# Kernel optimization log

Measured on AMD Instinct MI355X. Metric: run time of the kernel, lower is better.

## Reference

```python
import jax, jax.numpy as jnp
import numpy as np

N = 100000
E = 3200000
G = 64  # number of graphs in the batch


def gat_layer(x, edge_index, edge_attr, W, a_src, a_dst, We, a_e, b, n):
    """Single-head PyG GATConv with edge features.
    add_self_loops=True, fill_value='mean', negative_slope=0.2.
    Returns (out [n,C], new_edge_index [2,E+n], alpha [E+n,1])."""
    src, dst = edge_index[0], edge_index[1]
    # self-loop edge_attr = mean of incoming edge attrs (fill_value='mean')
    deg = jax.ops.segment_sum(jnp.ones_like(dst, dtype=edge_attr.dtype), dst, n)
    loop_attr = jax.ops.segment_sum(edge_attr, dst, n) / jnp.maximum(deg, 1.0)[:, None]
    loop = jnp.arange(n, dtype=src.dtype)
    src = jnp.concatenate([src, loop])
    dst = jnp.concatenate([dst, loop])
    ea = jnp.concatenate([edge_attr, loop_attr], axis=0)  # [E+n, edge_dim]
    h = x @ W                                             # [n, C]
    asrc = h @ a_src                                      # [n]
    adst = h @ a_dst                                      # [n]
    ae = (ea @ We) @ a_e                                  # [E+n]
    alpha = jax.nn.leaky_relu(asrc[src] + adst[dst] + ae, negative_slope=0.2)
    # segment softmax over destination nodes (every node has a self-loop)
    amax = jax.ops.segment_max(alpha, dst, n)
    ex = jnp.exp(alpha - amax[dst])
    denom = jax.ops.segment_sum(ex, dst, n)
    alpha = ex / (denom[dst] + 1e-16)
    out = jax.ops.segment_sum(alpha[:, None] * h[src], dst, n) + b
    return out, jnp.stack([src, dst]), alpha[:, None]


def setup_inputs() -> dict:
    key = jax.random.key(0)
    ks = jax.random.split(key, 24)
    s = 0.1
    inp = {
        "x": jax.random.normal(ks[0], (N, 5), jnp.float32),
        "edge_index": jax.random.randint(ks[1], (2, E), 0, N, jnp.int32),
        "edge_attr": jax.random.normal(ks[2], (E, 3), jnp.float32),
        "batch": jnp.sort(jax.random.randint(ks[3], (N,), 0, G, jnp.int32)),
        # conv1: in=5 -> 64, edge_dim=3
        "W1": jax.random.normal(ks[4], (5, 64), jnp.float32) * s,
        "as1": jax.random.normal(ks[5], (64,), jnp.float32) * s,
        "ad1": jax.random.normal(ks[6], (64,), jnp.float32) * s,
        "We1": jax.random.normal(ks[7], (3, 64), jnp.float32) * s,
        "ae1": jax.random.normal(ks[8], (64,), jnp.float32) * s,
        "b1": jnp.zeros((64,), jnp.float32),
        # conv2: 64 -> 64, edge_dim=1
        "W2": jax.random.normal(ks[9], (64, 64), jnp.float32) * s,
        "as2": jax.random.normal(ks[10], (64,), jnp.float32) * s,
        "ad2": jax.random.normal(ks[11], (64,), jnp.float32) * s,
        "We2": jax.random.normal(ks[12], (1, 64), jnp.float32) * s,
        "ae2": jax.random.normal(ks[13], (64,), jnp.float32) * s,
        "b2": jnp.zeros((64,), jnp.float32),
        # conv3: 64 -> 32, edge_dim=1
        "W3": jax.random.normal(ks[14], (64, 32), jnp.float32) * s,
        "as3": jax.random.normal(ks[15], (32,), jnp.float32) * s,
        "ad3": jax.random.normal(ks[16], (32,), jnp.float32) * s,
        "We3": jax.random.normal(ks[17], (1, 32), jnp.float32) * s,
        "ae3": jax.random.normal(ks[18], (32,), jnp.float32) * s,
        "b3": jnp.zeros((32,), jnp.float32),
    }
    return inp


def reference(x, edge_index, edge_attr, batch,
              W1, as1, ad1, We1, ae1, b1,
              W2, as2, ad2, We2, ae2, b2,
              W3, as3, ad3, We3, ae3, b3):
    h, ei, alpha = gat_layer(x, edge_index, edge_attr, W1, as1, ad1, We1, ae1, b1, N)
    h = jax.nn.relu(h)
    h, ei, alpha = gat_layer(h, ei, alpha, W2, as2, ad2, We2, ae2, b2, N)
    h = jax.nn.relu(h)
    h, _, _ = gat_layer(h, ei, alpha, W3, as3, ad3, We3, ae3, b3, N)
    # global mean pool over graphs
    cnt = jax.ops.segment_sum(jnp.ones((N,), h.dtype), batch, G)
    out = jax.ops.segment_sum(h, batch, G) / jnp.maximum(cnt, 1.0)[:, None]
    return out  # [G, 32]
```

## Files before the change

### kernel.cpp

```cpp
#include <hip/hip_runtime.h>
#include <hip/hip_fp16.h>

#define LRELU(x) ((x) > 0.f ? (x) : 0.2f * (x))
#define SBSH 9
#define SBN 512
#define NB1 256
#define MAXSB 1024
#define PC 16

__global__ void small_weights_k(const float* __restrict__ We1, const float* __restrict__ ae1,
                                const float* __restrict__ We2, const float* __restrict__ ae2,
                                const float* __restrict__ We3, const float* __restrict__ ae3,
                                float* __restrict__ sw) {
  int t = threadIdx.x;
  float v0 = We1[t] * ae1[t];
  float v1 = We1[64 + t] * ae1[t];
  float v2 = We1[128 + t] * ae1[t];
  float v3 = We2[t] * ae2[t];
  float v4 = (t < 32) ? We3[t] * ae3[t] : 0.f;
#pragma unroll
  for (int off = 32; off > 0; off >>= 1) {
    v0 += __shfl_down(v0, off);
    v1 += __shfl_down(v1, off);
    v2 += __shfl_down(v2, off);
    v3 += __shfl_down(v3, off);
    v4 += __shfl_down(v4, off);
  }
  if (t == 0) { sw[0] = v0; sw[1] = v1; sw[2] = v2; sw[3] = v3; sw[4] = v4; }
}

__global__ __launch_bounds__(256) void count1_k(const int* __restrict__ dst,
                                                int* __restrict__ gcnt, int E, int NSB) {
  __shared__ int cnt[MAXSB];
  const int t = threadIdx.x, blk = blockIdx.x;
  for (int i = t; i < NSB; i += 256) cnt[i] = 0;
  __syncthreads();
  const int CE = (E + NB1 - 1) / NB1;
  const int e0 = blk * CE, e1 = min(E, e0 + CE);
  for (int e = e0 + t; e < e1; e += 256) {
    int d = __builtin_nontemporal_load(&dst[e]);
    atomicAdd(&cnt[d >> SBSH], 1);
  }
  __syncthreads();
  for (int i = t; i < NSB; i += 256) gcnt[i * NB1 + blk] = cnt[i];
}

__global__ __launch_bounds__(1024) void scanA_k(const int* __restrict__ gcnt,
                                                int* __restrict__ gbase,
                                                int* __restrict__ bsum, int M) {
  __shared__ int s[1024];
  const int t = threadIdx.x;
  const int i = blockIdx.x * 1024 + t;
  int v = (i < M) ? gcnt[i] : 0;
  s[t] = v;
  __syncthreads();
  for (int off = 1; off < 1024; off <<= 1) {
    int add = (t >= off) ? s[t - off] : 0;
    __syncthreads();
    s[t] += add;
    __syncthreads();
  }
  if (i < M) gbase[i] = s[t] - v;
  if (t == 1023) bsum[blockIdx.x] = s[t];
}

__global__ void scanB_k(const int* __restrict__ bsum, int* __restrict__ boff, int nb) {
  if (threadIdx.x == 0) {
    int acc = 0;
    for (int b = 0; b < nb; b++) { boff[b] = acc; acc += bsum[b]; }
  }
}

__global__ void scanC_k(int* __restrict__ gbase, const int* __restrict__ boff,
                        int* __restrict__ rowptr, int M, int E) {
  int i = blockIdx.x * 256 + threadIdx.x;
  if (i < M) gbase[i] += boff[i >> 10];
  if (i == 0) { gbase[M] = E; rowptr[0] = 0; }
}

__global__ __launch_bounds__(256) void append2_k(
    const int* __restrict__ src, const int* __restrict__ dst,
    const float* __restrict__ eattr, const int* __restrict__ gbase,
    int2* __restrict__ recDS, const float* __restrict__ sw, int E, int NSB) {
  __shared__ int base[MAXSB];
  __shared__ int off[MAXSB];
  const int t = threadIdx.x, blk = blockIdx.x;
  for (int i = t; i < NSB; i += 256) { base[i] = gbase[i * NB1 + blk]; off[i] = 0; }
  __syncthreads();
  const float w0 = sw[0], w1 = sw[1], w2 = sw[2];
  const int CE = (E + NB1 - 1) / NB1;
  const int e0 = blk * CE, e1 = min(E, e0 + CE);
  for (int e = e0 + t; e < e1; e += 256) {
    int d = __builtin_nontemporal_load(&dst[e]);
    int sv = __builtin_nontemporal_load(&src[e]);
    float a0 = __builtin_nontemporal_load(&eattr[e * 3]);
    float a1 = __builtin_nontemporal_load(&eattr[e * 3 + 1]);
    float a2 = __builtin_nontemporal_load(&eattr[e * 3 + 2]);
    float ae = a0 * w0 + a1 * w1 + a2 * w2;
    int sb = d >> SBSH;
    int pos = base[sb] + atomicAdd(&off[sb], 1);
    recDS[pos] = make_int2((int)(((unsigned)(d & (SBN - 1)) << 23) | (unsigned)sv),
                           __float_as_int(ae));
  }
}

__global__ __launch_bounds__(1024) void sb_build_k(
    const int2* __restrict__ recDS, const int* __restrict__ gbase,
    const float* __restrict__ asrc, const float* __restrict__ adst,
    int* __restrict__ rowptr, float* __restrict__ asum, float* __restrict__ esum,
    int2* __restrict__ edge, int n, int NSB) {
  __shared__ int cnt[SBN];
  __shared__ int sc[SBN];
  __shared__ int fill[SBN];
  __shared__ float adl[SBN];
  __shared__ float rs[SBN];
  __shared__ float es[SBN];
  const int t = threadIdx.x, sb = blockIdx.x;
  const int v0 = sb << SBSH;
  const int nloc = min(SBN, n - v0);
  if (t < SBN) {
    cnt[t] = 0; fill[t] = 0; rs[t] = 0.f; es[t] = 0.f;
    adl[t] = (t < nloc) ? adst[v0 + t] : 0.f;
  }
  __syncthreads();
  const int seg0 = gbase[sb * NB1], seg1 = gbase[(sb + 1) * NB1];
  for (int i = seg0 + t; i < seg1; i += 1024)
    atomicAdd(&cnt[(unsigned)recDS[i].x >> 23], 1);
  __syncthreads();
  if (t < SBN) sc[t] = cnt[t];
  __syncthreads();
  for (int off = 1; off < SBN; off <<= 1) {
    int add = (t < SBN && t >= off) ? sc[t - off] : 0;
    __syncthreads();
    if (t < SBN) sc[t] += add;
    __syncthreads();
  }
  if (t < nloc) rowptr[v0 + t + 1] = seg0 + sc[t];
  for (int i = seg0 + t; i < seg1; i += 1024) {
    int2 rec = recDS[i];
    unsigned q = (unsigned)rec.x;
    float ae = __int_as_float(rec.y);
    int loc = q >> 23;
    int sv = (int)(q & 0x7FFFFFu);
    int pos = seg0 + (sc[loc] - cnt[loc]) + atomicAdd(&fill[loc], 1);
    float ex = __expf(LRELU(asrc[sv] + adl[loc] + ae));
    edge[pos] = make_int2(sv, __float_as_int(ex));
    atomicAdd(&rs[loc], ae);
    atomicAdd(&es[loc], ex);
  }
  __syncthreads();
  if (t < nloc) { asum[v0 + t] = rs[t]; esum[v0 + t] = es[t]; }
}


__global__ void gemm1_k(const float* __restrict__ x, const float* __restrict__ W,
                        const float* __restrict__ as, const float* __restrict__ ad,
                        __half* __restrict__ h, float* __restrict__ asrc,
                        float* __restrict__ adst, int n) {
  int lane = threadIdx.x & 63;
  int v = (blockIdx.x * blockDim.x + threadIdx.x) >> 6;
  if (v >= n) return;
  float acc = 0.f;
#pragma unroll
  for (int k = 0; k < 5; k++) acc += x[v * 5 + k] * W[k * 64 + lane];
  h[(size_t)v * 64 + lane] = __float2half(acc);
  float ps = acc * as[lane], pd = acc * ad[lane];
#pragma unroll
  for (int off = 32; off > 0; off >>= 1) {
    ps += __shfl_down(ps, off);
    pd += __shfl_down(pd, off);
  }
  if (lane == 0) { asrc[v] = ps; adst[v] = pd; }
}


template <int C>
__global__ __launch_bounds__(256) void gemm_tile_k(
    const __half* __restrict__ x, const float* __restrict__ W,
    const float* __restrict__ as, const float* __restrict__ ad,
    __half* __restrict__ h, float* __restrict__ asrc, float* __restrict__ adst, int n) {
  constexpr int NT = 4096 / C;
  constexpr int CG = C / 4;
  constexpr int XTP = NT + 4;
  __shared__ float XT[64][XTP];
  __shared__ float Wl[64 * C];
  const int t = threadIdx.x;
  const int v0 = blockIdx.x * NT;
  for (int i = t; i < 64 * C; i += 256) Wl[i] = W[i];
  for (int i = t; i < NT * 32; i += 256) {
    int node = i >> 5, kk = (i & 31) << 1;
    int v = v0 + node;
    unsigned u = (v < n) ? *(const unsigned*)&x[(size_t)v * 64 + kk] : 0u;
    float2 f = __half22float2(*(const __half2*)&u);
    XT[kk][node] = f.x;
    XT[kk + 1][node] = f.y;
  }
  __syncthreads();
  const int cg = t % CG, ng = t / CG;
  const int c0 = cg * 4, n0 = ng * 4;
  float acc[4][4] = {};
#pragma unroll 4
  for (int k = 0; k < 64; ++k) {
    const float4 xv = *(const float4*)&XT[k][n0];
    const float4 wv = *(const float4*)&Wl[k * C + c0];
    acc[0][0] += xv.x * wv.x; acc[0][1] += xv.x * wv.y; acc[0][2] += xv.x * wv.z; acc[0][3] += xv.x * wv.w;
    acc[1][0] += xv.y * wv.x; acc[1][1] += xv.y * wv.y; acc[1][2] += xv.y * wv.z; acc[1][3] += xv.y * wv.w;
    acc[2][0] += xv.z * wv.x; acc[2][1] += xv.z * wv.y; acc[2][2] += xv.z * wv.z; acc[2][3] += xv.z * wv.w;
    acc[3][0] += xv.w * wv.x; acc[3][1] += xv.w * wv.y; acc[3][2] += xv.w * wv.z; acc[3][3] += xv.w * wv.w;
  }
  float asv[4] = {as[c0], as[c0 + 1], as[c0 + 2], as[c0 + 3]};
  float adv[4] = {ad[c0], ad[c0 + 1], ad[c0 + 2], ad[c0 + 3]};
  float ps[4], pd[4];
#pragma unroll
  for (int ni = 0; ni < 4; ++ni) {
    ps[ni] = acc[ni][0] * asv[0] + acc[ni][1] * asv[1] + acc[ni][2] * asv[2] + acc[ni][3] * asv[3];
    pd[ni] = acc[ni][0] * adv[0] + acc[ni][1] * adv[1] + acc[ni][2] * adv[2] + acc[ni][3] * adv[3];
  }
#pragma unroll
  for (int off = CG / 2; off > 0; off >>= 1) {
#pragma unroll
    for (int ni = 0; ni < 4; ++ni) {
      ps[ni] += __shfl_xor(ps[ni], off);
      pd[ni] += __shfl_xor(pd[ni], off);
    }
  }
#pragma unroll
  for (int ni = 0; ni < 4; ++ni) {
    int v = v0 + n0 + ni;
    if (v < n) {
      union { __half hh[4]; uint2 u; } pk;
      pk.hh[0] = __float2half(acc[ni][0]);
      pk.hh[1] = __float2half(acc[ni][1]);
      pk.hh[2] = __float2half(acc[ni][2]);
      pk.hh[3] = __float2half(acc[ni][3]);
      *(uint2*)&h[(size_t)v * C + c0] = pk.u;
      if (cg == 0) { asrc[v] = ps[ni]; adst[v] = pd[ni]; }
    }
  }
}

__device__ __forceinline__ void fma8(float2* acc, float e, const uint4& u) {
  float2 f0 = __half22float2(*(const __half2*)&u.x);
  float2 f1 = __half22float2(*(const __half2*)&u.y);
  float2 f2 = __half22float2(*(const __half2*)&u.z);
  float2 f3 = __half22float2(*(const __half2*)&u.w);
  acc[0].x += e * f0.x; acc[0].y += e * f0.y;
  acc[1].x += e * f1.x; acc[1].y += e * f1.y;
  acc[2].x += e * f2.x; acc[2].y += e * f2.y;
  acc[3].x += e * f3.x; acc[3].y += e * f3.y;
}

template <int LAYER, int C>
__global__ __launch_bounds__(256) void agg_k(
    const int* __restrict__ rowptr, int2* __restrict__ edge,
    const __half* __restrict__ h, const float* __restrict__ asrc,
    const float* __restrict__ adst, const float* __restrict__ asum,
    const float* __restrict__ esum, const float* __restrict__ pinv,
    const float* __restrict__ lp1, const float* __restrict__ lp2,
    float* __restrict__ oinv, float* __restrict__ ol1, float* __restrict__ ol2,
    const float* __restrict__ sw, const float* __restrict__ bias,
    void* __restrict__ outv, int n) {
  constexpr int L = (C == 64) ? 64 : 32;
  constexpr int LPE = C / 8;
  constexpr int EPI = L / LPE;
  const int lane = threadIdx.x & 63;
  const int ln = lane & (L - 1);
  const int wid = (blockIdx.x * blockDim.x + threadIdx.x) >> 6;
  const int v = (C == 64) ? wid : wid * 2 + (lane >> 5);
  if (v >= n) return;
  const float s = (LAYER == 1) ? 1.f : (LAYER == 2 ? sw[3] : sw[4]);
  const float fac = (LAYER == 1) ? 1.f : pinv[v];
  const float sf = s * fac;
  const int r0 = rowptr[v], r1 = rowptr[v + 1];
  const float av_d = adst[v], av_s = asrc[v];

  float rawsum = 0.f, den = 0.f;
  if (LAYER >= 2) {
    for (int p = r0 + ln; p < r1; p += L) {
      int2 pk = edge[p];
      float a = __int_as_float(pk.y);
      rawsum += a;
      float lg = asrc[pk.x] + av_d + sf * a;
      float ex = __expf(LRELU(lg));
      edge[p].y = __float_as_int(ex);
      den += ex;
    }
    __threadfence_block();
#pragma unroll
    for (int off = L / 2; off > 0; off >>= 1) {
      den += __shfl_xor(den, off);
      rawsum += __shfl_xor(rawsum, off);
    }
  } else {
    den = esum[v];
  }
  const float base = av_s + av_d;
  float la1 = 0.f, la2 = 0.f, e1 = 0.f, e2 = 0.f;
  if (LAYER >= 2) { la1 = fac * lp1[v]; e1 = __expf(LRELU(base + s * la1)); den += e1; }
  if (LAYER >= 3) { la2 = fac * lp2[v]; e2 = __expf(LRELU(base + s * la2)); den += e2; }
  int dd = (r1 - r0) + (LAYER - 1);
  if (dd < 1) dd = 1;
  float sum_a = (LAYER == 1) ? asum[v] : fac * rawsum + la1 + la2;
  float lmean = sum_a / (float)dd;
  float exm = __expf(LRELU(base + s * lmean));
  den += exm;
  float inv = 1.f / (den + 1e-16f);
  if (ln == 0) {
    if (LAYER < 3) oinv[v] = inv;
    if (LAYER == 1) ol1[v] = exm;
    if (LAYER == 2) { ol1[v] = e1; ol2[v] = exm; }
  }

  const int g = ln / LPE;
  const int q = ln % LPE;
  const uint4* __restrict__ h4 = (const uint4*)h;
  float2 accA[4] = {{0.f,0.f},{0.f,0.f},{0.f,0.f},{0.f,0.f}};
  float2 accB[4] = {{0.f,0.f},{0.f,0.f},{0.f,0.f},{0.f,0.f}};
  int p = r0;
  for (; p + 2 * EPI <= r1; p += 2 * EPI) {
    int2 rA = edge[p + g];
    int2 rB = edge[p + EPI + g];
    uint4 uA = h4[rA.x * LPE + q];
    uint4 uB = h4[rB.x * LPE + q];
    fma8(accA, __int_as_float(rA.y), uA);
    fma8(accB, __int_as_float(rB.y), uB);
  }
  for (; p < r1; p += EPI) {
    int idx = p + g;
    float e_;
    int2 rr;
    if (idx < r1) { rr = edge[idx]; e_ = __int_as_float(rr.y); }
    else { rr = edge[r1 - 1]; e_ = 0.f; }
    uint4 u = h4[rr.x * LPE + q];
    fma8(accA, e_, u);
  }
#pragma unroll
  for (int j = 0; j < 4; ++j) {
    accA[j].x += accB[j].x;
    accA[j].y += accB[j].y;
  }
#pragma unroll
  for (int off = LPE; off < L; off <<= 1) {
#pragma unroll
    for (int j = 0; j < 4; ++j) {
      accA[j].x += __shfl_xor(accA[j].x, off);
      accA[j].y += __shfl_xor(accA[j].y, off);
    }
  }
  if (g == 0) {
    uint4 uh = h4[v * LPE + q];
    float2 f0 = __half22float2(*(const __half2*)&uh.x);
    float2 f1 = __half22float2(*(const __half2*)&uh.y);
    float2 f2 = __half22float2(*(const __half2*)&uh.z);
    float2 f3 = __half22float2(*(const __half2*)&uh.w);
    float sl = e1 + e2 + exm;
    float o[8];
    o[0] = (accA[0].x + sl * f0.x) * inv + bias[q * 8 + 0];
    o[1] = (accA[0].y + sl * f0.y) * inv + bias[q * 8 + 1];
    o[2] = (accA[1].x + sl * f1.x) * inv + bias[q * 8 + 2];
    o[3] = (accA[1].y + sl * f1.y) * inv + bias[q * 8 + 3];
    o[4] = (accA[2].x + sl * f2.x) * inv + bias[q * 8 + 4];
    o[5] = (accA[2].y + sl * f2.y) * inv + bias[q * 8 + 5];
    o[6] = (accA[3].x + sl * f3.x) * inv + bias[q * 8 + 6];
    o[7] = (accA[3].y + sl * f3.y) * inv + bias[q * 8 + 7];
    if (LAYER < 3) {
      union { __half hh[8]; uint4 u; } pk;
#pragma unroll
      for (int j = 0; j < 8; ++j) pk.hh[j] = __float2half(fmaxf(o[j], 0.f));
      *(uint4*)&((__half*)outv)[(size_t)v * C + q * 8] = pk.u;
    } else {
      float4 o0 = make_float4(o[0], o[1], o[2], o[3]);
      float4 o1 = make_float4(o[4], o[5], o[6], o[7]);
      *(float4*)&((float*)outv)[(size_t)v * C + q * 8] = o0;
      *(float4*)&((float*)outv)[(size_t)v * C + q * 8 + 4] = o1;
    }
  }
}


__global__ __launch_bounds__(256) void poolA_k(const float* __restrict__ h,
                                               const int* __restrict__ batch,
                                               float* __restrict__ partial, int n) {
  const int b = blockIdx.x;
  const int g = b / PC, ch = b % PC;
  int lo = 0, hi = n;
  while (lo < hi) { int m = (lo + hi) >> 1; if (batch[m] < g) lo = m + 1; else hi = m; }
  const int start = lo;
  hi = n;
  while (lo < hi) { int m = (lo + hi) >> 1; if (batch[m] < g + 1) lo = m + 1; else hi = m; }
  const int end = lo;
  const int len = end - start;
  const int c0 = start + (int)((long long)len * ch / PC);
  const int c1 = start + (int)((long long)len * (ch + 1) / PC);
  const int t = threadIdx.x;
  const int c = t & 31, r = t >> 5;
  float acc = 0.f;
  for (int v = c0 + r; v < c1; v += 8) acc += h[(size_t)v * 32 + c];
  __shared__ float sm[256];
  sm[t] = acc;
  __syncthreads();
  if (t < 128) sm[t] += sm[t + 128];
  __syncthreads();
  if (t < 64) sm[t] += sm[t + 64];
  __syncthreads();
  if (t < 32) partial[(b << 5) + t] = sm[t] + sm[t + 32];
}

__global__ void poolB_k(const float* __restrict__ partial, const int* __restrict__ batch,
                        float* __restrict__ out, int n) {
  const int g = blockIdx.x;
  const int t = threadIdx.x;
  if (t >= 32) return;
  int lo = 0, hi = n;
  while (lo < hi) { int m = (lo + hi) >> 1; if (batch[m] < g) lo = m + 1; else hi = m; }
  const int start = lo;
  hi = n;
  while (lo < hi) { int m = (lo + hi) >> 1; if (batch[m] < g + 1) lo = m + 1; else hi = m; }
  const int cnt = lo - start;
  float acc = 0.f;
#pragma unroll
  for (int ch = 0; ch < PC; ++ch) acc += partial[((g * PC + ch) << 5) + t];
  out[g * 32 + t] = acc / (float)(cnt > 0 ? cnt : 1);
}


extern "C" void kernel_launch(void* const* d_in, const int* in_sizes, int n_in,
                              void* d_out, int out_size, void* d_ws, size_t ws_size,
                              hipStream_t stream) {
  const float* x     = (const float*)d_in[0];
  const int*   ei    = (const int*)d_in[1];
  const float* eattr = (const float*)d_in[2];
  const int*   batch = (const int*)d_in[3];
  const float *W1 = (const float*)d_in[4],  *as1 = (const float*)d_in[5],
              *ad1 = (const float*)d_in[6], *We1 = (const float*)d_in[7],
              *ae1 = (const float*)d_in[8], *b1  = (const float*)d_in[9];
  const float *W2 = (const float*)d_in[10], *as2 = (const float*)d_in[11],
              *ad2 = (const float*)d_in[12], *We2 = (const float*)d_in[13],
              *ae2 = (const float*)d_in[14], *b2  = (const float*)d_in[15];
  const float *W3 = (const float*)d_in[16], *as3 = (const float*)d_in[17],
              *ad3 = (const float*)d_in[18], *We3 = (const float*)d_in[19],
              *ae3 = (const float*)d_in[20], *b3  = (const float*)d_in[21];

  const int n = in_sizes[3];
  const int E = in_sizes[1] / 2;
  const int G = out_size / 32;
  const int* srcp = ei;
  const int* dstp = ei + E;
  const int NSB = (n + SBN - 1) >> SBSH;
  const int M = NSB * NB1;
  const int NBL = (M + 1023) / 1024;

  char* w = (char*)d_ws;
  auto alloc = [&](size_t bytes) -> void* {
    void* p = (void*)w;
    w += (bytes + 255) & ~(size_t)255;
    return p;
  };
  size_t oh_bytes = ((size_t)n * 128 + 255) & ~(size_t)255;
  size_t blob_sz = (size_t)E * 8;
  if (blob_sz < oh_bytes + (size_t)n * 128) blob_sz = oh_bytes + (size_t)n * 128;
  char* blob = (char*)alloc(blob_sz);
  int2*   recDS = (int2*)blob;
  __half* Oh    = (__half*)blob;
  float*  O32   = (float*)(blob + oh_bytes);
  int2*  edge  = (int2*)alloc((size_t)E * 8);
  __half* H    = (__half*)alloc((size_t)n * 64 * 2);
  int*   gcnt  = (int*)alloc((size_t)M * 4);
  int*   gbase = (int*)alloc((size_t)(M + 1) * 4);
  int*   bsum  = (int*)alloc((size_t)NBL * 4 + 256);
  int*   boff  = (int*)alloc((size_t)NBL * 4 + 256);
  int*   rowptr= (int*)alloc((size_t)(n + 1) * 4);
  float* asum  = (float*)alloc((size_t)n * 4);
  float* esum  = (float*)alloc((size_t)n * 4);
  float* asrcB = (float*)alloc((size_t)n * 4);
  float* adstB = (float*)alloc((size_t)n * 4);
  float* loopA = (float*)alloc((size_t)n * 4);
  float* loopB1= (float*)alloc((size_t)n * 4);
  float* loopB2= (float*)alloc((size_t)n * 4);
  float* invA  = (float*)alloc((size_t)n * 4);
  float* invB  = (float*)alloc((size_t)n * 4);
  float* sw    = (float*)alloc(256);
  float* part  = (float*)alloc((size_t)G * PC * 32 * 4);

  dim3 blk256(256);
  dim3 gWave((n + 3) / 4);
  const int nw3 = (n + 1) / 2;
  dim3 gWave3((nw3 + 3) / 4);

  small_weights_k<<<1, 64, 0, stream>>>(We1, ae1, We2, ae2, We3, ae3, sw);
  count1_k<<<NB1, blk256, 0, stream>>>(dstp, gcnt, E, NSB);
  scanA_k<<<NBL, 1024, 0, stream>>>(gcnt, gbase, bsum, M);
  scanB_k<<<1, 64, 0, stream>>>(bsum, boff, NBL);
  scanC_k<<<dim3((M + 256) / 256), blk256, 0, stream>>>(gbase, boff, rowptr, M, E);
  append2_k<<<NB1, blk256, 0, stream>>>(srcp, dstp, eattr, gbase, recDS, sw, E, NSB);
  gemm1_k<<<gWave, blk256, 0, stream>>>(x, W1, as1, ad1, H, asrcB, adstB, n);
  sb_build_k<<<NSB, 1024, 0, stream>>>(recDS, gbase, asrcB, adstB,
                                       rowptr, asum, esum, edge, n, NSB);
  agg_k<1, 64><<<gWave, blk256, 0, stream>>>(rowptr, edge, H, asrcB, adstB, asum, esum,
                                             nullptr, nullptr, nullptr,
                                             invA, loopA, nullptr, sw, b1, (void*)Oh, n);
  gemm_tile_k<64><<<dim3((n + 63) / 64), blk256, 0, stream>>>(Oh, W2, as2, ad2, H, asrcB, adstB, n);
  agg_k<2, 64><<<gWave, blk256, 0, stream>>>(rowptr, edge, H, asrcB, adstB, nullptr, nullptr,
                                             invA, loopA, nullptr,
                                             invB, loopB1, loopB2, sw, b2, (void*)Oh, n);
  gemm_tile_k<32><<<dim3((n + 127) / 128), blk256, 0, stream>>>(Oh, W3, as3, ad3, H, asrcB, adstB, n);
  agg_k<3, 32><<<gWave3, blk256, 0, stream>>>(rowptr, edge, H, asrcB, adstB, nullptr, nullptr,
                                              invB, loopB1, loopB2,
                                              nullptr, nullptr, nullptr, sw, b3, (void*)O32, n);
  poolA_k<<<dim3(G * PC), blk256, 0, stream>>>(O32, batch, part, n);
  poolB_k<<<G, 64, 0, stream>>>(part, batch, (float*)d_out, n);
}
```

Baseline: 413.3 us.

## Compute rowptr via global per-node degree scan; unroll aggregation loop by three

Per-destination degrees are now counted with global atomics in the append pass and prefix-summed by a separate scan, so rowptr is known before sb_build. This removes the per-superblock count pass over recDS and the shared-memory scan in sb_build. In exchange it adds 3.2M global atomics on a 100K-entry array, a zeroing kernel and three extra scan launches. The aggregation gather loop is also unrolled to three edges per iteration to raise memory-level parallelism.

```diff
diff --git a/kernel.cpp b/kernel.cpp
--- a/kernel.cpp
+++ b/kernel.cpp
@@ -29,6 +29,11 @@
   if (t == 0) { sw[0] = v0; sw[1] = v1; sw[2] = v2; sw[3] = v3; sw[4] = v4; }
 }
 
+__global__ void zero_deg_k(int* __restrict__ deg, int m) {
+  int i = blockIdx.x * 256 + threadIdx.x;
+  if (i < m) deg[i] = 0;
+}
+
 __global__ __launch_bounds__(256) void count1_k(const int* __restrict__ dst,
                                                 int* __restrict__ gcnt, int E, int NSB) {
   __shared__ int cnt[MAXSB];
@@ -45,13 +50,13 @@
   for (int i = t; i < NSB; i += 256) gcnt[i * NB1 + blk] = cnt[i];
 }
 
-__global__ __launch_bounds__(1024) void scanA_k(const int* __restrict__ gcnt,
-                                                int* __restrict__ gbase,
+__global__ __launch_bounds__(1024) void scanA_k(const int* __restrict__ in,
+                                                int* __restrict__ out,
                                                 int* __restrict__ bsum, int M) {
   __shared__ int s[1024];
   const int t = threadIdx.x;
   const int i = blockIdx.x * 1024 + t;
-  int v = (i < M) ? gcnt[i] : 0;
+  int v = (i < M) ? in[i] : 0;
   s[t] = v;
   __syncthreads();
   for (int off = 1; off < 1024; off <<= 1) {
@@ -60,7 +65,7 @@
     s[t] += add;
     __syncthreads();
   }
-  if (i < M) gbase[i] = s[t] - v;
+  if (i < M) out[i] = s[t] - v;
   if (t == 1023) bsum[blockIdx.x] = s[t];
 }
 
@@ -71,17 +76,23 @@
   }
 }
 
-__global__ void scanC_k(int* __restrict__ gbase, const int* __restrict__ boff,
-                        int* __restrict__ rowptr, int M, int E) {
+__global__ void scanC_gbase_k(int* __restrict__ gbase, const int* __restrict__ boff,
+                              int M, int E) {
   int i = blockIdx.x * 256 + threadIdx.x;
   if (i < M) gbase[i] += boff[i >> 10];
-  if (i == 0) { gbase[M] = E; rowptr[0] = 0; }
+  if (i == 0) gbase[M] = E;
+}
+
+__global__ void scanC_plain_k(int* __restrict__ arr, const int* __restrict__ boff, int M) {
+  int i = blockIdx.x * 256 + threadIdx.x;
+  if (i < M) arr[i] += boff[i >> 10];
 }
 
 __global__ __launch_bounds__(256) void append2_k(
     const int* __restrict__ src, const int* __restrict__ dst,
     const float* __restrict__ eattr, const int* __restrict__ gbase,
-    int2* __restrict__ recDS, const float* __restrict__ sw, int E, int NSB) {
+    int2* __restrict__ recDS, int* __restrict__ deg,
+    const float* __restrict__ sw, int E, int NSB) {
   __shared__ int base[MAXSB];
   __shared__ int off[MAXSB];
   const int t = threadIdx.x, blk = blockIdx.x;
@@ -98,6 +109,7 @@
     float a2 = __builtin_nontemporal_load(&eattr[e * 3 + 2]);
     float ae = a0 * w0 + a1 * w1 + a2 * w2;
     int sb = d >> SBSH;
+    atomicAdd(&deg[d], 1);
     int pos = base[sb] + atomicAdd(&off[sb], 1);
     recDS[pos] = make_int2((int)(((unsigned)(d & (SBN - 1)) << 23) | (unsigned)sv),
                            __float_as_int(ae));
@@ -106,11 +118,10 @@
 
 __global__ __launch_bounds__(1024) void sb_build_k(
     const int2* __restrict__ recDS, const int* __restrict__ gbase,
-    const float* __restrict__ asrc, const float* __restrict__ adst,
-    int* __restrict__ rowptr, float* __restrict__ asum, float* __restrict__ esum,
-    int2* __restrict__ edge, int n, int NSB) {
-  __shared__ int cnt[SBN];
-  __shared__ int sc[SBN];
+    const int* __restrict__ rowptr, const float* __restrict__ asrc,
+    const float* __restrict__ adst, float* __restrict__ asum,
+    float* __restrict__ esum, int2* __restrict__ edge, int n, int NSB) {
+  __shared__ int basev[SBN];
   __shared__ int fill[SBN];
   __shared__ float adl[SBN];
   __shared__ float rs[SBN];
@@ -119,30 +130,19 @@
   const int v0 = sb << SBSH;
   const int nloc = min(SBN, n - v0);
   if (t < SBN) {
-    cnt[t] = 0; fill[t] = 0; rs[t] = 0.f; es[t] = 0.f;
+    fill[t] = 0; rs[t] = 0.f; es[t] = 0.f;
+    basev[t] = (t < nloc) ? rowptr[v0 + t] : 0;
     adl[t] = (t < nloc) ? adst[v0 + t] : 0.f;
   }
   __syncthreads();
   const int seg0 = gbase[sb * NB1], seg1 = gbase[(sb + 1) * NB1];
-  for (int i = seg0 + t; i < seg1; i += 1024)
-    atomicAdd(&cnt[(unsigned)recDS[i].x >> 23], 1);
-  __syncthreads();
-  if (t < SBN) sc[t] = cnt[t];
-  __syncthreads();
-  for (int off = 1; off < SBN; off <<= 1) {
-    int add = (t < SBN && t >= off) ? sc[t - off] : 0;
-    __syncthreads();
-    if (t < SBN) sc[t] += add;
-    __syncthreads();
-  }
-  if (t < nloc) rowptr[v0 + t + 1] = seg0 + sc[t];
   for (int i = seg0 + t; i < seg1; i += 1024) {
     int2 rec = recDS[i];
     unsigned q = (unsigned)rec.x;
     float ae = __int_as_float(rec.y);
     int loc = q >> 23;
     int sv = (int)(q & 0x7FFFFFu);
-    int pos = seg0 + (sc[loc] - cnt[loc]) + atomicAdd(&fill[loc], 1);
+    int pos = basev[loc] + atomicAdd(&fill[loc], 1);
     float ex = __expf(LRELU(asrc[sv] + adl[loc] + ae));
     edge[pos] = make_int2(sv, __float_as_int(ex));
     atomicAdd(&rs[loc], ae);
@@ -317,20 +317,26 @@
   float2 accA[4] = {{0.f,0.f},{0.f,0.f},{0.f,0.f},{0.f,0.f}};
   float2 accB[4] = {{0.f,0.f},{0.f,0.f},{0.f,0.f},{0.f,0.f}};
   int p = r0;
-  for (; p + 2 * EPI <= r1; p += 2 * EPI) {
+  for (; p + 3 * EPI <= r1; p += 3 * EPI) {
     int2 rA = edge[p + g];
     int2 rB = edge[p + EPI + g];
+    int2 rC = edge[p + 2 * EPI + g];
     uint4 uA = h4[rA.x * LPE + q];
     uint4 uB = h4[rB.x * LPE + q];
+    uint4 uC = h4[rC.x * LPE + q];
     fma8(accA, __int_as_float(rA.y), uA);
     fma8(accB, __int_as_float(rB.y), uB);
-  }
-  for (; p < r1; p += EPI) {
+    fma8(accA, __int_as_float(rC.y), uC);
+  }
+  for (; p + EPI <= r1; p += EPI) {
+    int2 rr = edge[p + g];
+    uint4 u = h4[rr.x * LPE + q];
+    fma8(accA, __int_as_float(rr.y), u);
+  }
+  if (p < r1) {
     int idx = p + g;
-    float e_;
-    int2 rr;
-    if (idx < r1) { rr = edge[idx]; e_ = __int_as_float(rr.y); }
-    else { rr = edge[r1 - 1]; e_ = 0.f; }
+    int2 rr = (idx < r1) ? edge[idx] : edge[r1 - 1];
+    float e_ = (idx < r1) ? __int_as_float(rr.y) : 0.f;
     uint4 u = h4[rr.x * LPE + q];
     fma8(accA, e_, u);
   }
@@ -449,6 +455,8 @@
   const int NSB = (n + SBN - 1) >> SBSH;
   const int M = NSB * NB1;
   const int NBL = (M + 1023) / 1024;
+  const int M2 = n + 1;
+  const int NBL2 = (M2 + 1023) / 1024;
 
   char* w = (char*)d_ws;
   auto alloc = [&](size_t bytes) -> void* {
@@ -469,7 +477,10 @@
   int*   gbase = (int*)alloc((size_t)(M + 1) * 4);
   int*   bsum  = (int*)alloc((size_t)NBL * 4 + 256);
   int*   boff  = (int*)alloc((size_t)NBL * 4 + 256);
+  int*   deg   = (int*)alloc((size_t)M2 * 4);
   int*   rowptr= (int*)alloc((size_t)(n + 1) * 4);
+  int*   bsum2 = (int*)alloc((size_t)NBL2 * 4 + 256);
+  int*   boff2 = (int*)alloc((size_t)NBL2 * 4 + 256);
   float* asum  = (float*)alloc((size_t)n * 4);
   float* esum  = (float*)alloc((size_t)n * 4);
   float* asrcB = (float*)alloc((size_t)n * 4);
@@ -488,14 +499,18 @@
   dim3 gWave3((nw3 + 3) / 4);
 
   small_weights_k<<<1, 64, 0, stream>>>(We1, ae1, We2, ae2, We3, ae3, sw);
+  zero_deg_k<<<dim3((M2 + 255) / 256), blk256, 0, stream>>>(deg, M2);
   count1_k<<<NB1, blk256, 0, stream>>>(dstp, gcnt, E, NSB);
   scanA_k<<<NBL, 1024, 0, stream>>>(gcnt, gbase, bsum, M);
   scanB_k<<<1, 64, 0, stream>>>(bsum, boff, NBL);
-  scanC_k<<<dim3((M + 256) / 256), blk256, 0, stream>>>(gbase, boff, rowptr, M, E);
-  append2_k<<<NB1, blk256, 0, stream>>>(srcp, dstp, eattr, gbase, recDS, sw, E, NSB);
+  scanC_gbase_k<<<dim3((M + 255) / 256), blk256, 0, stream>>>(gbase, boff, M, E);
+  append2_k<<<NB1, blk256, 0, stream>>>(srcp, dstp, eattr, gbase, recDS, deg, sw, E, NSB);
+  scanA_k<<<NBL2, 1024, 0, stream>>>(deg, rowptr, bsum2, M2);
+  scanB_k<<<1, 64, 0, stream>>>(bsum2, boff2, NBL2);
+  scanC_plain_k<<<dim3((M2 + 255) / 256), blk256, 0, stream>>>(rowptr, boff2, M2);
   gemm1_k<<<gWave, blk256, 0, stream>>>(x, W1, as1, ad1, H, asrcB, adstB, n);
-  sb_build_k<<<NSB, 1024, 0, stream>>>(recDS, gbase, asrcB, adstB,
-                                       rowptr, asum, esum, edge, n, NSB);
+  sb_build_k<<<NSB, 1024, 0, stream>>>(recDS, gbase, rowptr, asrcB, adstB,
+                                       asum, esum, edge, n, NSB);
   agg_k<1, 64><<<gWave, blk256, 0, stream>>>(rowptr, edge, H, asrcB, adstB, asum, esum,
                                              nullptr, nullptr, nullptr,
                                              invA, loopA, nullptr, sw, b1, (void*)Oh, n);
```

Measured after the change: 520.4 us. 1.26x slower.
